# Kernel optimization log

Measured on AMD Instinct MI355X. Metric: run time of the kernel, lower is better.

The kernel has to match this reference:

```python
import jax, jax.numpy as jnp
import numpy as np

# hyperparameters from init_kwargs
STEPSZ = 0.1
ALPHA = 0.01
BETA = 0.01
NSTEPS = 50
DMAX = 15.0
EXTGRADFAC = 10.0
B, H, W, N = 2, 256, 256, 128


def _bilerp(field, pts):
    # field: [H, W]; pts: [N, 2] as (row, col) float coords -> [N]
    h, w = field.shape
    y = jnp.clip(pts[:, 0], 0.0, h - 1.001)
    x = jnp.clip(pts[:, 1], 0.0, w - 1.001)
    y0 = jnp.floor(y).astype(jnp.int32)
    x0 = jnp.floor(x).astype(jnp.int32)
    y1 = y0 + 1
    x1 = x0 + 1
    wy = y - y0.astype(field.dtype)
    wx = x - x0.astype(field.dtype)
    return (field[y0, x0] * (1 - wy) * (1 - wx)
            + field[y0, x1] * (1 - wy) * wx
            + field[y1, x0] * wy * (1 - wx)
            + field[y1, x1] * wy * wx)


def _evolve(pred, nodes):
    # pred: [H, W] distance-map prediction; nodes: [N, 2] closed-contour points
    gy = jnp.gradient(pred, axis=0)
    gx = jnp.gradient(pred, axis=1)
    hi = jnp.array([pred.shape[0] - 1.0, pred.shape[1] - 1.0], dtype=pred.dtype)

    def step(x, _):
        # internal forces: 2nd derivative (elasticity) and 4th derivative (rigidity)
        d2 = jnp.roll(x, -1, 0) + jnp.roll(x, 1, 0) - 2.0 * x
        d4 = jnp.roll(d2, -1, 0) + jnp.roll(d2, 1, 0) - 2.0 * d2
        # external force: descend the predicted distance map
        ext = -EXTGRADFAC * jnp.stack([_bilerp(gy, x), _bilerp(gx, x)], axis=-1)
        x = x + STEPSZ * (ALPHA * d2 - BETA * d4 + ext)
        x = jnp.clip(x, 0.0, hi)
        return x, None

    x, _ = jax.lax.scan(step, nodes, None, length=NSTEPS)
    return x


def _render(nodes):
    # distance from every pixel to the nearest snake segment, clamped at DMAX
    yy, xx = jnp.meshgrid(jnp.arange(H, dtype=nodes.dtype),
                          jnp.arange(W, dtype=nodes.dtype), indexing='ij')
    q = jnp.stack([yy, xx], axis=-1).reshape(-1, 2)          # [P, 2]
    p0 = nodes                                               # [N, 2]
    p1 = jnp.roll(nodes, -1, 0)                              # closed contour
    d = p1 - p0                                              # [N, 2]
    dd = jnp.sum(d * d, axis=-1) + 1e-8                      # [N]
    qp = q[:, None, :] - p0[None, :, :]                      # [P, N, 2]
    t = jnp.clip(jnp.sum(qp * d[None], axis=-1) / dd, 0.0, 1.0)  # [P, N]
    r = qp - t[..., None] * d[None]                          # residual to projection
    dist = jnp.sqrt(jnp.sum(r * r, axis=-1) + 1e-12)         # [P, N]
    return jnp.minimum(dist.min(axis=1), DMAX).reshape(H, W)


def setup_inputs() -> dict:
    key = jax.random.key(0)
    k1, k2 = jax.random.split(key)
    pred_dmap = jax.random.normal(k1, (B, 1, H, W), dtype=jnp.float32)
    # snake control points spread over the image
    nodes = jax.random.uniform(k2, (B, N, 2), dtype=jnp.float32) * (H - 1.0)
    return {"pred_dmap": pred_dmap, "nodes": nodes}


def reference(pred_dmap, nodes):
    pred = pred_dmap[:, 0]                                   # [B, H, W] (detached in torch)
    final_nodes = jax.vmap(_evolve)(jax.lax.stop_gradient(pred), nodes)
    snake_dm = jax.vmap(_render)(final_nodes)[:, None]       # [B, 1, H, W]
    snake_dm = jax.lax.stop_gradient(snake_dm)               # noGrad: snake path detached
    loss = jnp.mean(jnp.square(pred_dmap - snake_dm))
    return loss
```

## Files before the change

kernel.cpp:

```cpp
#include <hip/hip_runtime.h>

#define HH 256
#define WW 256
#define NB 2
#define NN 128
#define NSTEPS_K 50
#define NBLK 256
#define MAGIC_G 0x11C0FFEE
#define MAGIC_E 0x22C0FFEE
#define MAGIC_R 0x33C0FFEE
#define SPIN_G 400000
#define SPIN_E 120000
#define SPIN_R 120000

#define WS_PART   0
#define WS_GFLG   256
#define WS_RFLG   512
#define WS_EREP   1024
#define WS_FNODE  2048
#define WS_FIELD  4096
#define WS_NEEDED_BYTES ((WS_FIELD + (size_t)NB * HH * WW * 2) * 4)

static __device__ __forceinline__ int ld_i(int* p) {
    return __hip_atomic_load(p, __ATOMIC_RELAXED, __HIP_MEMORY_SCOPE_AGENT);
}
static __device__ __forceinline__ void st_i(int* p, int v) {
    __hip_atomic_store(p, v, __ATOMIC_RELAXED, __HIP_MEMORY_SCOPE_AGENT);
}
static __device__ __forceinline__ unsigned long long ld_u64(unsigned long long* p) {
    return __hip_atomic_load(p, __ATOMIC_RELAXED, __HIP_MEMORY_SCOPE_AGENT);
}
static __device__ __forceinline__ void st_u64(unsigned long long* p, unsigned long long v) {
    __hip_atomic_store(p, v, __ATOMIC_RELAXED, __HIP_MEMORY_SCOPE_AGENT);
}
static __device__ __forceinline__ float ld_f(float* p) {
    return __hip_atomic_load(p, __ATOMIC_RELAXED, __HIP_MEMORY_SCOPE_AGENT);
}
static __device__ __forceinline__ void st_f(float* p, float v) {
    __hip_atomic_store(p, v, __ATOMIC_RELAXED, __HIP_MEMORY_SCOPE_AGENT);
}
union F2U { float2 f2; unsigned long long u; };

typedef float f4v __attribute__((ext_vector_type(4)));
static __device__ __forceinline__ f4v ld_pair(const float2* p) {
    f4v r;
    __builtin_memcpy(&r, p, sizeof(f4v));
    return r;
}

__global__ __launch_bounds__(1024) void fused3_kernel(
        const float* __restrict__ pred,
        const float* __restrict__ nodes_in,
        float* __restrict__ ws,
        float* __restrict__ out) {
    float* partials = ws + WS_PART;
    int*   g_flags  = (int*)(ws + WS_GFLG);
    int*   r_flags  = (int*)(ws + WS_RFLG);
    int*   e_rep    = (int*)(ws + WS_EREP);
    unsigned long long* fnodes_u = (unsigned long long*)(ws + WS_FNODE);
    unsigned long long* field_u  = (unsigned long long*)(ws + WS_FIELD);
    const float2*       field_f2 = (const float2*)(ws + WS_FIELD);

    const int blk = blockIdx.x;
    const int tid = threadIdx.x;
    const int myBatch = blk >> 7;

    if (tid < 512) {
        int idx = blk * 512 + tid;
        int b = idx >> 16, p = idx & 0xFFFF;
        int i = p >> 8, j = p & (WW - 1);
        const float* f = pred + (b << 16);
        int iu = max(i - 1, 0), id = min(i + 1, HH - 1);
        int jl = max(j - 1, 0), jr = min(j + 1, WW - 1);
        float sy = (i == 0 || i == HH - 1) ? 1.0f : 0.5f;
        float sx = (j == 0 || j == WW - 1) ? 1.0f : 0.5f;
        F2U cv;
        cv.f2 = make_float2(sy * (f[(id << 8) + j] - f[(iu << 8) + j]),
                            sx * (f[(i << 8) + jr] - f[(i << 8) + jl]));
        st_u64(&field_u[idx], cv.u);
    }
    __syncthreads();
    if (tid == 0) st_i(&g_flags[blk], MAGIC_G);

    if (blk < NB) {
        const int b = blk;
        const float2* gb = field_f2 + (b << 16);

        {
            const int w = tid >> 6, ln = tid & 63;
            float acc = 0.0f;
            #pragma unroll
            for (int k = 0; k < 8; ++k) {
                int* fl = &g_flags[b * 128 + k * 16 + w];
                for (int it = 0; it < SPIN_G; ++it) {
                    if (ld_i(fl) == MAGIC_G) break;
                    __builtin_amdgcn_s_sleep(1);
                }
                acc += gb[(k * 1024 + w * 64 + ln) << 3].x;
            }
            asm volatile("" :: "v"(acc));
        }
        __syncthreads();

        if (tid < 64) {
            const int l = tid;
            const int pl = (l + 63) & 63;
            const int nl = (l + 1) & 63;
            float4 nd = ((const float4*)nodes_in)[b * 64 + l];
            float y0n = nd.x, x0n = nd.y;
            float y1n = nd.z, x1n = nd.w;

            __builtin_amdgcn_s_setprio(1);
            for (int s = 0; s < NSTEPS_K; ++s) {
                float yca = fminf(fmaxf(y0n, 0.0f), 254.999f);
                float xca = fminf(fmaxf(x0n, 0.0f), 254.999f);
                int ra = (int)yca, ca = (int)xca;
                float wya = yca - (float)ra, wxa = xca - (float)ca;
                int basea = (ra << 8) + ca;
                f4v ra0 = ld_pair(&gb[basea]);
                f4v ra1 = ld_pair(&gb[basea + WW]);

                float ycb = fminf(fmaxf(y1n, 0.0f), 254.999f);
                float xcb = fminf(fmaxf(x1n, 0.0f), 254.999f);
                int rb = (int)ycb, cb = (int)xcb;
                float wyb = ycb - (float)rb, wxb = xcb - (float)cb;
                int baseb = (rb << 8) + cb;
                f4v rb0 = ld_pair(&gb[baseb]);
                f4v rb1 = ld_pair(&gb[baseb + WW]);

                float pya = __shfl(y0n, pl), pxa = __shfl(x0n, pl);
                float pyb = __shfl(y1n, pl), pxb = __shfl(x1n, pl);
                float nya = __shfl(y0n, nl), nxa = __shfl(x0n, nl);
                float nyb = __shfl(y1n, nl), nxb = __shfl(x1n, nl);

                float d2ya = (y1n + pyb) - 2.0f * y0n;
                float d2xa = (x1n + pxb) - 2.0f * x0n;
                float d2yb = (nya + y0n) - 2.0f * y1n;
                float d2xb = (nxa + x0n) - 2.0f * x1n;
                float d2pyb = (y0n + pya) - 2.0f * pyb;
                float d2pxb = (x0n + pxa) - 2.0f * pxb;
                float d2nya = (nyb + y1n) - 2.0f * nya;
                float d2nxa = (nxb + x1n) - 2.0f * nxa;

                float d4ya = (d2yb + d2pyb) - 2.0f * d2ya;
                float d4xa = (d2xb + d2pxb) - 2.0f * d2xa;
                float d4yb = (d2nya + d2ya) - 2.0f * d2yb;
                float d4xb = (d2nxa + d2xa) - 2.0f * d2xb;

                float ua = 1.0f - wya, va = 1.0f - wxa;
                float bya = ra0[0] * ua * va + ra0[2] * ua * wxa + ra1[0] * wya * va + ra1[2] * wya * wxa;
                float bxa = ra0[1] * ua * va + ra0[3] * ua * wxa + ra1[1] * wya * va + ra1[3] * wya * wxa;
                float ub = 1.0f - wyb, vb = 1.0f - wxb;
                float byb = rb0[0] * ub * vb + rb0[2] * ub * wxb + rb1[0] * wyb * vb + rb1[2] * wyb * wxb;
                float bxb = rb0[1] * ub * vb + rb0[3] * ub * wxb + rb1[1] * wyb * vb + rb1[3] * wyb * wxb;

                y0n = y0n + 0.1f * ((0.01f * d2ya - 0.01f * d4ya) + (-10.0f * bya));
                x0n = x0n + 0.1f * ((0.01f * d2xa - 0.01f * d4xa) + (-10.0f * bxa));
                y1n = y1n + 0.1f * ((0.01f * d2yb - 0.01f * d4yb) + (-10.0f * byb));
                x1n = x1n + 0.1f * ((0.01f * d2xb - 0.01f * d4xb) + (-10.0f * bxb));
                y0n = fminf(fmaxf(y0n, 0.0f), 255.0f);
                x0n = fminf(fmaxf(x0n, 0.0f), 255.0f);
                y1n = fminf(fmaxf(y1n, 0.0f), 255.0f);
                x1n = fminf(fmaxf(x1n, 0.0f), 255.0f);
            }
            __builtin_amdgcn_s_setprio(0);

            F2U c0, c1;
            c0.f2 = make_float2(y0n, x0n);
            c1.f2 = make_float2(y1n, x1n);
            st_u64(&fnodes_u[b * 128 + 2 * l], c0.u);
            st_u64(&fnodes_u[b * 128 + 2 * l + 1], c1.u);
            asm volatile("s_waitcnt vmcnt(0)" ::: "memory");
            if (l == 0) {
                #pragma unroll
                for (int k = 0; k < 8; ++k) st_i(&e_rep[(b * 8 + k) * 64], MAGIC_E);
            }
        }
        __syncthreads();
    }

    if (tid == 0) {
        int* rep = &e_rep[(myBatch * 8 + (blk & 7)) * 64];
        for (int it = 0; it < SPIN_E; ++it) {
            if (ld_i(rep) == MAGIC_E) break;
            __builtin_amdgcn_s_sleep(8);
        }
    }
    __syncthreads();

    __shared__ float nny[NN], nnx[NN];
    __shared__ float p0y[NN], p0x[NN], sdy[NN], sdx[NN], sidd[NN];
    if (tid < NN) {
        F2U cv; cv.u = ld_u64(&fnodes_u[myBatch * 128 + tid]);
        nny[tid] = cv.f2.x; nnx[tid] = cv.f2.y;
    }
    __syncthreads();
    if (tid < NN) {
        float ay = nny[tid], ax = nnx[tid];
        int j = (tid + 1) & (NN - 1);
        float cy = nny[j], cx = nnx[j];
        float ddy = cy - ay, ddx = cx - ax;
        p0y[tid] = ay; p0x[tid] = ax;
        sdy[tid] = ddy; sdx[tid] = ddx;
        sidd[tid] = 1.0f / (ddy * ddy + ddx * ddx + 1e-8f);
    }
    __syncthreads();

    float se = 0.0f;
    if (tid < 512) {
        int pixin = (blk & 127) * 512 + tid;
        float qy = (float)(pixin >> 8);
        float qx = (float)(pixin & (WW - 1));
        float minr2 = 1e30f;
        #pragma unroll 8
        for (int s = 0; s < NN; ++s) {
            float qpy = qy - p0y[s];
            float qpx = qx - p0x[s];
            float t = (qpy * sdy[s] + qpx * sdx[s]) * sidd[s];
            t = fminf(fmaxf(t, 0.0f), 1.0f);
            float ry = qpy - t * sdy[s];
            float rx = qpx - t * sdx[s];
            minr2 = fminf(minr2, ry * ry + rx * rx);
        }
        float dist = fminf(sqrtf(minr2 + 1e-12f), 15.0f);
        float e = pred[(myBatch << 16) + pixin] - dist;
        se = e * e;
    }
    for (int off = 32; off > 0; off >>= 1) se += __shfl_down(se, off);
    __shared__ float red[16];
    if ((tid & 63) == 0) red[tid >> 6] = se;
    __syncthreads();
    if (tid == 0) {
        float p = 0.0f;
        #pragma unroll
        for (int w = 0; w < 8; ++w) p += red[w];
        st_f(&partials[blk], p);
        asm volatile("s_waitcnt vmcnt(0)" ::: "memory");
        st_i(&r_flags[blk], MAGIC_R);
    }

    if (blk == 0 && tid < 64) {
        for (int it = 0; it < SPIN_R; ++it) {
            bool ok = (ld_i(&r_flags[tid*4+0]) == MAGIC_R) &&
                      (ld_i(&r_flags[tid*4+1]) == MAGIC_R) &&
                      (ld_i(&r_flags[tid*4+2]) == MAGIC_R) &&
                      (ld_i(&r_flags[tid*4+3]) == MAGIC_R);
            if (__all(ok)) break;
            __builtin_amdgcn_s_sleep(8);
        }
        float s = 0.0f;
        #pragma unroll
        for (int k = 0; k < 4; ++k)
            s += ld_f(&partials[tid + (k << 6)]);
        for (int off = 32; off > 0; off >>= 1) s += __shfl_down(s, off);
        if (tid == 0) out[0] = s * (1.0f / (float)(NB * HH * WW));
        #pragma unroll
        for (int k = 0; k < 4; ++k) { st_i(&g_flags[tid*4+k], 0); st_i(&r_flags[tid*4+k], 0); }
        if (tid < 16) st_i(&e_rep[tid * 64], 0);
    }
}

__device__ __forceinline__ void sample_grad_direct(const float* __restrict__ f,
                                                   float y, float x,
                                                   float& by, float& bx) {
    float yc = fminf(fmaxf(y, 0.0f), 254.999f);
    float xc = fminf(fmaxf(x, 0.0f), 254.999f);
    int r0 = (int)yc, c0 = (int)xc;
    int r1 = r0 + 1, c1 = c0 + 1;
    float wy = yc - (float)r0, wx = xc - (float)c0;
    int rm = max(r0 - 1, 0), rp = min(r1 + 1, HH - 1);
    int cm = max(c0 - 1, 0), cp = min(c1 + 1, WW - 1);
    float sy0 = (r0 == 0) ? 1.0f : 0.5f;
    float sy1 = (r1 == HH - 1) ? 1.0f : 0.5f;
    float sx0 = (c0 == 0) ? 1.0f : 0.5f;
    float sx1 = (c1 == WW - 1) ? 1.0f : 0.5f;
    const float* fr0 = f + (r0 << 8);
    const float* fr1 = f + (r1 << 8);
    const float* frm = f + (rm << 8);
    const float* frp = f + (rp << 8);
    float f00 = fr0[c0], f01 = fr0[c1];
    float f10 = fr1[c0], f11 = fr1[c1];
    float f0m = fr0[cm], f0p = fr0[cp];
    float f1m = fr1[cm], f1p = fr1[cp];
    float fm0 = frm[c0], fm1 = frm[c1];
    float fp0 = frp[c0], fp1 = frp[c1];
    float gy00 = sy0 * (f10 - fm0), gy01 = sy0 * (f11 - fm1);
    float gy10 = sy1 * (fp0 - f00), gy11 = sy1 * (fp1 - f01);
    float gx00 = sx0 * (f01 - f0m), gx01 = sx1 * (f0p - f00);
    float gx10 = sx0 * (f11 - f1m), gx11 = sx1 * (f1p - f10);
    float u = 1.0f - wy, v = 1.0f - wx;
    by = gy00 * u * v + gy01 * u * wx + gy10 * wy * v + gy11 * wy * wx;
    bx = gx00 * u * v + gx01 * u * wx + gx10 * wy * v + gx11 * wy * wx;
}

__global__ __launch_bounds__(64, 1) void evolve_direct_kernel(
        const float* __restrict__ pred,
        const float* __restrict__ nodes_in,
        float* __restrict__ nodes_out,
        int* __restrict__ counter) {
    const int b = blockIdx.x;
    const int l = threadIdx.x;
    if (b == 0 && l == 0)
        __hip_atomic_store(counter, 0, __ATOMIC_RELAXED, __HIP_MEMORY_SCOPE_AGENT);
    const float* f = pred + b * HH * WW;
    const int pl = (l + 63) & 63;
    const int nl = (l + 1) & 63;
    float4 nd = ((const float4*)nodes_in)[b * 64 + l];
    float y0n = nd.x, x0n = nd.y, y1n = nd.z, x1n = nd.w;
    for (int s = 0; s < NSTEPS_K; ++s) {
        float by0, bx0, by1, bx1;
        sample_grad_direct(f, y0n, x0n, by0, bx0);
        sample_grad_direct(f, y1n, x1n, by1, bx1);
        float pya = __shfl(y0n, pl), pxa = __shfl(x0n, pl);
        float pyb = __shfl(y1n, pl), pxb = __shfl(x1n, pl);
        float nya = __shfl(y0n, nl), nxa = __shfl(x0n, nl);
        float nyb = __shfl(y1n, nl), nxb = __shfl(x1n, nl);
        float d2ya = (y1n + pyb) - 2.0f * y0n;
        float d2xa = (x1n + pxb) - 2.0f * x0n;
        float d2yb = (nya + y0n) - 2.0f * y1n;
        float d2xb = (nxa + x0n) - 2.0f * x1n;
        float d2pyb = (y0n + pya) - 2.0f * pyb;
        float d2pxb = (x0n + pxa) - 2.0f * pxb;
        float d2nya = (nyb + y1n) - 2.0f * nya;
        float d2nxa = (nxb + x1n) - 2.0f * nxa;
        float d4ya = (d2yb + d2pyb) - 2.0f * d2ya;
        float d4xa = (d2xb + d2pxb) - 2.0f * d2xa;
        float d4yb = (d2nya + d2ya) - 2.0f * d2yb;
        float d4xb = (d2nxa + d2xa) - 2.0f * d2xb;
        y0n = y0n + 0.1f * ((0.01f * d2ya - 0.01f * d4ya) + (-10.0f * by0));
        x0n = x0n + 0.1f * ((0.01f * d2xa - 0.01f * d4xa) + (-10.0f * bx0));
        y1n = y1n + 0.1f * ((0.01f * d2yb - 0.01f * d4yb) + (-10.0f * by1));
        x1n = x1n + 0.1f * ((0.01f * d2xb - 0.01f * d4xb) + (-10.0f * bx1));
        y0n = fminf(fmaxf(y0n, 0.0f), 255.0f);
        x0n = fminf(fmaxf(x0n, 0.0f), 255.0f);
        y1n = fminf(fmaxf(y1n, 0.0f), 255.0f);
        x1n = fminf(fmaxf(x1n, 0.0f), 255.0f);
    }
    float4 o4; o4.x = y0n; o4.y = x0n; o4.z = y1n; o4.w = x1n;
    ((float4*)nodes_out)[b * 64 + l] = o4;
}

#define RBLK ((HH * WW) / 256)
#define NPART (NB * RBLK)

__global__ void render_kernel(const float* __restrict__ pred,
                              const float* __restrict__ nodes,
                              float* __restrict__ partials,
                              int* __restrict__ counter,
                              float* __restrict__ out) {
    const int b = blockIdx.y;
    const int chunk = blockIdx.x;
    const int tid = threadIdx.x;
    __shared__ float p0y[NN], p0x[NN], sdy[NN], sdx[NN], sidd[NN];
    if (tid < NN) {
        float ay = nodes[(b * NN + tid) * 2 + 0];
        float ax = nodes[(b * NN + tid) * 2 + 1];
        int j = (tid + 1) & (NN - 1);
        float cy = nodes[(b * NN + j) * 2 + 0];
        float cx = nodes[(b * NN + j) * 2 + 1];
        float ddy = cy - ay, ddx = cx - ax;
        p0y[tid] = ay; p0x[tid] = ax;
        sdy[tid] = ddy; sdx[tid] = ddx;
        sidd[tid] = 1.0f / (ddy * ddy + ddx * ddx + 1e-8f);
    }
    __syncthreads();
    const int pix = chunk * 256 + tid;
    const float qy = (float)(pix >> 8);
    const float qx = (float)(pix & (WW - 1));
    float minr2 = 1e30f;
#pragma unroll 8
    for (int s = 0; s < NN; ++s) {
        float qpy = qy - p0y[s];
        float qpx = qx - p0x[s];
        float t = (qpy * sdy[s] + qpx * sdx[s]) * sidd[s];
        t = fminf(fmaxf(t, 0.0f), 1.0f);
        float ry = qpy - t * sdy[s];
        float rx = qpx - t * sdx[s];
        minr2 = fminf(minr2, ry * ry + rx * rx);
    }
    float dist = fminf(sqrtf(minr2 + 1e-12f), 15.0f);
    float e = pred[b * HH * WW + pix] - dist;
    float se = e * e;
    for (int off = 32; off > 0; off >>= 1) se += __shfl_down(se, off);
    __shared__ float red[4];
    if ((tid & 63) == 0) red[tid >> 6] = se;
    __syncthreads();
    __shared__ int lastBlk;
    if (tid == 0) {
        float p = (red[0] + red[1]) + (red[2] + red[3]);
        __hip_atomic_store(&partials[b * RBLK + chunk], p, __ATOMIC_RELEASE, __HIP_MEMORY_SCOPE_AGENT);
        int t = __hip_atomic_fetch_add(counter, 1, __ATOMIC_ACQ_REL, __HIP_MEMORY_SCOPE_AGENT);
        lastBlk = (t == NPART - 1);
    }
    __syncthreads();
    if (lastBlk) {
        float v = __hip_atomic_load(&partials[tid], __ATOMIC_RELAXED, __HIP_MEMORY_SCOPE_AGENT)
                + __hip_atomic_load(&partials[tid + 256], __ATOMIC_RELAXED, __HIP_MEMORY_SCOPE_AGENT);
        for (int off = 32; off > 0; off >>= 1) v += __shfl_down(v, off);
        __shared__ float red2[4];
        if ((tid & 63) == 0) red2[tid >> 6] = v;
        __syncthreads();
        if (tid == 0)
            out[0] = ((red2[0] + red2[1]) + (red2[2] + red2[3])) * (1.0f / (float)(NB * HH * WW));
    }
}

extern "C" void kernel_launch(void* const* d_in, const int* in_sizes, int n_in,
                              void* d_out, int out_size, void* d_ws, size_t ws_size,
                              hipStream_t stream) {
    const float* pred = (const float*)d_in[0];
    const float* nodes = (const float*)d_in[1];
    float* ws = (float*)d_ws;

    if (ws_size >= WS_NEEDED_BYTES) {
        fused3_kernel<<<dim3(NBLK), dim3(1024), 0, stream>>>(pred, nodes, ws, (float*)d_out);
    } else {
        float* partials = ws;
        float* fnodes = ws + 512;
        int* counter = (int*)(ws + 1024);
        evolve_direct_kernel<<<dim3(NB), dim3(64), 0, stream>>>(pred, nodes, fnodes, counter);
        render_kernel<<<dim3(RBLK, NB), dim3(256), 0, stream>>>(pred, fnodes, partials,
                                                                counter, (float*)d_out);
    }
}
```

Before: 47.09 us.

## Prefetch gradient field into evolving block's XCC L2 via co-located helper blocks

New measurement: 43.97 us, median of 2. 1.07x faster.

```diff
diff --git a/kernel.cpp b/kernel.cpp
--- a/kernel.cpp
+++ b/kernel.cpp
@@ -9,6 +9,7 @@
 #define MAGIC_G 0x11C0FFEE
 #define MAGIC_E 0x22C0FFEE
 #define MAGIC_R 0x33C0FFEE
+#define MAGIC_X 0x5EC0DE00
 #define SPIN_G 400000
 #define SPIN_E 120000
 #define SPIN_R 120000
@@ -17,7 +18,8 @@
 #define WS_GFLG   256
 #define WS_RFLG   512
 #define WS_EREP   1024
-#define WS_FNODE  2048
+#define WS_XCC    2048
+#define WS_FNODE  2112
 #define WS_FIELD  4096
 #define WS_NEEDED_BYTES ((WS_FIELD + (size_t)NB * HH * WW * 2) * 4)
 
@@ -48,7 +50,13 @@
     return r;
 }
 
-__global__ __launch_bounds__(1024) void fused3_kernel(
+static __device__ __forceinline__ int read_xcc() {
+    int xr;
+    asm volatile("s_getreg_b32 %0, hwreg(HW_REG_XCC_ID)" : "=s"(xr));
+    return xr & 0xFF;
+}
+
+__global__ __launch_bounds__(1024) void fused4_kernel(
         const float* __restrict__ pred,
         const float* __restrict__ nodes_in,
         float* __restrict__ ws,
@@ -57,6 +65,7 @@
     int*   g_flags  = (int*)(ws + WS_GFLG);
     int*   r_flags  = (int*)(ws + WS_RFLG);
     int*   e_rep    = (int*)(ws + WS_EREP);
+    int*   xcc_pub  = (int*)(ws + WS_XCC);
     unsigned long long* fnodes_u = (unsigned long long*)(ws + WS_FNODE);
     unsigned long long* field_u  = (unsigned long long*)(ws + WS_FIELD);
     const float2*       field_f2 = (const float2*)(ws + WS_FIELD);
@@ -64,6 +73,8 @@
     const int blk = blockIdx.x;
     const int tid = threadIdx.x;
     const int myBatch = blk >> 7;
+
+    if (blk < NB && tid == 0) st_i(&xcc_pub[blk], MAGIC_X | read_xcc());
 
     if (tid < 512) {
         int idx = blk * 512 + tid;
@@ -82,23 +93,59 @@
     __syncthreads();
     if (tid == 0) st_i(&g_flags[blk], MAGIC_G);
 
+    if (blk >= NB) {
+        const int myxcc = read_xcc();
+        __shared__ int s_pub[NB];
+        if (tid == 0) {
+            #pragma unroll
+            for (int b = 0; b < NB; ++b) {
+                int pub = 0;
+                for (int it = 0; it < 50000; ++it) {
+                    pub = ld_i(&xcc_pub[b]);
+                    if ((pub & (int)0xFFFFFF00) == MAGIC_X) break;
+                    __builtin_amdgcn_s_sleep(1);
+                }
+                s_pub[b] = pub;
+            }
+        }
+        __syncthreads();
+        #pragma unroll
+        for (int b = 0; b < NB; ++b) {
+            int pub = s_pub[b];
+            if ((pub & (int)0xFFFFFF00) == MAGIC_X && (pub & 0xFF) == myxcc) {
+                const int rank = (blk >> 3) & 31;
+                if (tid == 0) {
+                    #pragma unroll
+                    for (int k = 0; k < 4; ++k) {
+                        int* fl = &g_flags[b * 128 + rank * 4 + k];
+                        for (int it = 0; it < SPIN_G; ++it) {
+                            if (ld_i(fl) == MAGIC_G) break;
+                            __builtin_amdgcn_s_sleep(1);
+                        }
+                    }
+                }
+                __syncthreads();
+                if (tid < 256) {
+                    int line = rank * 256 + tid;
+                    float v = field_f2[(b << 16) + (line << 3)].x;
+                    asm volatile("" :: "v"(v));
+                }
+            }
+        }
+    }
+
     if (blk < NB) {
         const int b = blk;
         const float2* gb = field_f2 + (b << 16);
 
-        {
-            const int w = tid >> 6, ln = tid & 63;
-            float acc = 0.0f;
-            #pragma unroll
-            for (int k = 0; k < 8; ++k) {
-                int* fl = &g_flags[b * 128 + k * 16 + w];
-                for (int it = 0; it < SPIN_G; ++it) {
-                    if (ld_i(fl) == MAGIC_G) break;
-                    __builtin_amdgcn_s_sleep(1);
-                }
-                acc += gb[(k * 1024 + w * 64 + ln) << 3].x;
+        if (tid < 64) {
+            int f0 = b * 128 + tid * 2;
+            for (int it = 0; it < SPIN_G; ++it) {
+                bool ok = (ld_i(&g_flags[f0]) == MAGIC_G) &&
+                          (ld_i(&g_flags[f0 + 1]) == MAGIC_G);
+                if (__all(ok)) break;
+                __builtin_amdgcn_s_sleep(1);
             }
-            asm volatile("" :: "v"(acc));
         }
         __syncthreads();
 
@@ -257,6 +304,7 @@
         #pragma unroll
         for (int k = 0; k < 4; ++k) { st_i(&g_flags[tid*4+k], 0); st_i(&r_flags[tid*4+k], 0); }
         if (tid < 16) st_i(&e_rep[tid * 64], 0);
+        if (tid < NB) st_i(&xcc_pub[tid], 0);
     }
 }
 
@@ -413,7 +461,7 @@
     float* ws = (float*)d_ws;
 
     if (ws_size >= WS_NEEDED_BYTES) {
-        fused3_kernel<<<dim3(NBLK), dim3(1024), 0, stream>>>(pred, nodes, ws, (float*)d_out);
+        fused4_kernel<<<dim3(NBLK), dim3(1024), 0, stream>>>(pred, nodes, ws, (float*)d_out);
     } else {
         float* partials = ws;
         float* fnodes = ws + 512;
```
